# Optimization experiments

Hardware: AMD Instinct MI355X
Metric: run time of the kernel (lower is better)

## Reference

```python
import jax, jax.numpy as jnp
import numpy as np

N = 100000      # nodes
E = 1600000     # edges (avg degree 16)
D_IN, D_H, D_OUT = 100, 256, 47
EPS = 1e-5


def setup_inputs() -> dict:
    key = jax.random.key(0)
    ks = jax.random.split(key, 10)
    w = lambda k, s: jax.random.normal(k, s, jnp.float32) * 0.02
    return {
        "x": jax.random.normal(ks[0], (N, D_IN), jnp.float32),
        "edge_index": jax.random.randint(ks[1], (2, E), 0, N),
        # SAGEConv 0: lin_l (aggregated neighbors, has bias), lin_r (root, no bias)
        "wl0": w(ks[2], (D_IN, D_H)), "wr0": w(ks[3], (D_IN, D_H)), "b0": jnp.zeros((D_H,), jnp.float32),
        "g0": jnp.ones((D_H,), jnp.float32), "be0": jnp.zeros((D_H,), jnp.float32),
        # SAGEConv 1
        "wl1": w(ks[4], (D_H, D_H)), "wr1": w(ks[5], (D_H, D_H)), "b1": jnp.zeros((D_H,), jnp.float32),
        "g1": jnp.ones((D_H,), jnp.float32), "be1": jnp.zeros((D_H,), jnp.float32),
        # SAGEConv 2 (output)
        "wl2": w(ks[6], (D_H, D_OUT)), "wr2": w(ks[7], (D_H, D_OUT)), "b2": jnp.zeros((D_OUT,), jnp.float32),
    }


def _sage_conv(x, src, dst, wl, wr, b):
    # mean aggregation of source-node features onto destination nodes
    agg = jax.ops.segment_sum(x[src], dst, num_segments=N)          # [N, d_in]
    cnt = jax.ops.segment_sum(jnp.ones((src.shape[0],), x.dtype), dst, num_segments=N)
    mean = agg / jnp.maximum(cnt, 1.0)[:, None]                     # 0 in-degree -> 0
    return mean @ wl + x @ wr + b


def _bn(h, gamma, beta):
    m = h.mean(axis=0)
    v = h.var(axis=0)
    return (h - m) * jax.lax.rsqrt(v + EPS) * gamma + beta


def reference(x, edge_index, wl0, wr0, b0, g0, be0, wl1, wr1, b1, g1, be1, wl2, wr2, b2):
    src, dst = edge_index[0], edge_index[1]
    h = jax.nn.relu(_bn(_sage_conv(x, src, dst, wl0, wr0, b0), g0, be0))
    h = jax.nn.relu(_bn(_sage_conv(h, src, dst, wl1, wr1, b1), g1, be1))
    h = _sage_conv(h, src, dst, wl2, wr2, b2)
    return jax.nn.log_softmax(h, axis=1)
```

## Files before the change

### kernel.cpp

```cpp
#include <hip/hip_runtime.h>
#include <hip/hip_bf16.h>
#include <math.h>

#define DEVFN __device__ __forceinline__

typedef unsigned int uint32;
typedef unsigned short ushort_t;

using bf16x8 = __attribute__((ext_vector_type(8))) short;
using f32x4  = __attribute__((ext_vector_type(4))) float;
using f32x2  = __attribute__((ext_vector_type(2))) float;

DEVFN float bf2f(ushort_t u) {
    union { uint32 i; float f; } v; v.i = ((uint32)u) << 16; return v.f;
}
DEVFN float asf(uint32 u) {
    union { uint32 i; float f; } v; v.i = u; return v.f;
}
DEVFN ushort_t f2bf(float f) {
    union { float f; uint32 i; } v; v.f = f;
    uint32 u = v.i;
    uint32 r = (u + 0x7FFFu + ((u >> 16) & 1u)) >> 16;
    return (ushort_t)r;
}

DEVFN void gload_lds16(const void* g, void* l) {
    __builtin_amdgcn_global_load_lds(
        (const __attribute__((address_space(1))) void*)g,
        (__attribute__((address_space(3))) void*)l, 16, 0, 0);
}

__global__ void k_cast_x(const float* __restrict__ x, ushort_t* __restrict__ xb, int N) {
    int total = N * 128;
    for (int i = blockIdx.x * blockDim.x + threadIdx.x; i < total; i += gridDim.x * blockDim.x) {
        int col = i & 127, row = i >> 7;
        float v = (col < 100) ? x[row * 100 + col] : 0.f;
        xb[i] = f2bf(v);
    }
}

DEVFN void cast_one(const float* __restrict__ w, ushort_t* __restrict__ wt,
                    int j, int K, int Nout, int Kp) {
    int k = j % Kp, n = j / Kp;
    float v = (k < K && n < Nout) ? w[k * Nout + n] : 0.f;
    wt[j] = f2bf(v);
}

__global__ void k_cast_wall(const float* __restrict__ wl0, const float* __restrict__ wr0,
                            const float* __restrict__ wl1, const float* __restrict__ wr1,
                            const float* __restrict__ wl2, const float* __restrict__ wr2,
                            ushort_t* __restrict__ wlt0, ushort_t* __restrict__ wrt0,
                            ushort_t* __restrict__ wlt1, ushort_t* __restrict__ wrt1,
                            ushort_t* __restrict__ wcat2) {
    const int total = 229376;
    for (int i = blockIdx.x * blockDim.x + threadIdx.x; i < total; i += gridDim.x * blockDim.x) {
        int j = i;
        if (j < 32768)        cast_one(wl0, wlt0, j, 100, 256, 128);
        else if (j < 65536)   cast_one(wr0, wrt0, j - 32768, 100, 256, 128);
        else if (j < 131072)  cast_one(wl1, wlt1, j - 65536, 256, 256, 256);
        else if (j < 196608)  cast_one(wr1, wrt1, j - 131072, 256, 256, 256);
        else if (j < 212992)  cast_one(wl2, wcat2, j - 196608, 256, 47, 256);
        else                  cast_one(wr2, wcat2 + 16384, j - 212992, 256, 47, 256);
    }
}

__global__ void k_bincount(const int* __restrict__ dst, int E, int CH, int nbins, int nblk,
                           int* __restrict__ binCnt) {
    __shared__ int scnt[128];
    int blk = blockIdx.x, tid = threadIdx.x;
    for (int b = tid; b < 128; b += 256) scnt[b] = 0;
    __syncthreads();
    int e0 = blk * CH, e1 = min(E, e0 + CH);
    for (int i = e0 + tid; i < e1; i += 256)
        atomicAdd(&scnt[dst[i] >> 10], 1);
    __syncthreads();
    for (int b = tid; b < nbins; b += 256) binCnt[b * nblk + blk] = scnt[b];
}

__global__ void k_blocksum(const int* __restrict__ v, int n, int* __restrict__ bsum) {
    __shared__ int s[1024];
    int i = blockIdx.x * 1024 + threadIdx.x;
    s[threadIdx.x] = (i < n) ? v[i] : 0;
    __syncthreads();
    for (int o = 512; o > 0; o >>= 1) {
        if (threadIdx.x < o) s[threadIdx.x] += s[threadIdx.x + o];
        __syncthreads();
    }
    if (threadIdx.x == 0) bsum[blockIdx.x] = s[0];
}

__global__ void k_scanb(int* __restrict__ bsum, int NB) {
    if (blockIdx.x == 0 && threadIdx.x == 0) {
        int acc = 0;
        for (int i = 0; i < NB; ++i) { int v = bsum[i]; bsum[i] = acc; acc += v; }
    }
}

__global__ void k_exscan(const int* __restrict__ v, const int* __restrict__ bsum,
                         int n, int* __restrict__ outOff) {
    __shared__ int s[1024];
    int t = threadIdx.x;
    int i = blockIdx.x * 1024 + t;
    int val = (i < n) ? v[i] : 0;
    s[t] = val;
    __syncthreads();
    for (int o = 1; o < 1024; o <<= 1) {
        int add = (t >= o) ? s[t - o] : 0;
        __syncthreads();
        s[t] += add;
        __syncthreads();
    }
    if (i < n) outOff[i] = s[t] - val + bsum[blockIdx.x];
}

__global__ void k_binscatter(const int* __restrict__ src, const int* __restrict__ dst,
                             int E, int CH, int nbins, int nblk,
                             const int* __restrict__ binOff, int* __restrict__ ebin) {
    __shared__ int scur[128];
    int blk = blockIdx.x, tid = threadIdx.x;
    for (int b = tid; b < nbins; b += 256) scur[b] = binOff[b * nblk + blk];
    __syncthreads();
    int e0 = blk * CH, e1 = min(E, e0 + CH);
    for (int i = e0 + tid; i < e1; i += 256) {
        int d = dst[i];
        int b = d >> 10;
        int pos = atomicAdd(&scur[b], 1);
        ebin[pos] = (src[i] << 10) | (d & 1023);
    }
}

__global__ void k_bincsr(const int* __restrict__ ebin, const int* __restrict__ binOff,
                         int E, int N, int nbins, int nblk,
                         int* __restrict__ poffs, int* __restrict__ deg, int* __restrict__ csr2) {
    __shared__ int sdeg[1024];
    __shared__ int scur[1024];
    int bin = blockIdx.x, t = threadIdx.x;
    int binStart = binOff[bin * nblk];
    int binEnd = (bin + 1 < nbins) ? binOff[(bin + 1) * nblk] : E;
    int pbase = ((binStart + 15) & ~15) + bin * 15376;
    sdeg[t] = 0;
    __syncthreads();
    for (int i = binStart + t; i < binEnd; i += 1024)
        atomicAdd(&sdeg[ebin[i] & 1023], 1);
    __syncthreads();
    int v = sdeg[t];
    int pv = (v + 15) & ~15;
    sdeg[t] = pv;
    __syncthreads();
    for (int o = 1; o < 1024; o <<= 1) {
        int add = (t >= o) ? sdeg[t - o] : 0;
        __syncthreads();
        sdeg[t] += add;
        __syncthreads();
    }
    int pex = sdeg[t] - pv;
    int node = bin * 1024 + t;
    if (node < N) { poffs[node] = pbase + pex; deg[node] = v; }
    scur[t] = pex;
    __syncthreads();
    for (int i = binStart + t; i < binEnd; i += 1024) {
        int e = ebin[i];
        int slot = atomicAdd(&scur[e & 1023], 1);
        csr2[pbase + slot] = e >> 10;
    }
    for (int j = v; j < pv; ++j) csr2[pbase + pex + j] = N;
}

template <int D>
__global__ __launch_bounds__(256) void k_agg(
    const ushort_t* __restrict__ h, const int* __restrict__ poffs,
    const int* __restrict__ deg, const int* __restrict__ csr2,
    int N, ushort_t* __restrict__ mean) {
    constexpr int LPR = D / 8;
    constexpr int EPG = 64 / LPR;
    constexpr int STEP = 4 * EPG;
    int wid = (blockIdx.x * blockDim.x + threadIdx.x) >> 6;
    int lane = threadIdx.x & 63;
    if (wid >= N) return;
    const int seg = lane % LPR, sub = lane / LPR;
    int off = poffs[wid], cnt = deg[wid];
    int pcnt = (cnt + 15) & ~15;
    f32x2 acc[4] = {};
    const ushort_t* hp = h + seg * 8;
    int4 idx = *(const int4*)(csr2 + off + sub * 4);
    for (int b = 0; b < pcnt; b += STEP) {
        uint4 d0 = *(const uint4*)(hp + (size_t)idx.x * D);
        uint4 d1 = *(const uint4*)(hp + (size_t)idx.y * D);
        uint4 d2 = *(const uint4*)(hp + (size_t)idx.z * D);
        uint4 d3 = *(const uint4*)(hp + (size_t)idx.w * D);
        int4 idxn = *(const int4*)(csr2 + off + b + STEP + sub * 4);
        uint32 dd[16] = {d0.x, d0.y, d0.z, d0.w, d1.x, d1.y, d1.z, d1.w,
                         d2.x, d2.y, d2.z, d2.w, d3.x, d3.y, d3.z, d3.w};
#pragma unroll
        for (int q = 0; q < 16; ++q) {
            f32x2 tv;
            tv.x = asf(dd[q] << 16);
            tv.y = asf(dd[q] & 0xffff0000u);
            acc[q & 3] += tv;
        }
        idx = idxn;
    }
    float a[8] = {acc[0].x, acc[0].y, acc[1].x, acc[1].y,
                  acc[2].x, acc[2].y, acc[3].x, acc[3].y};
#pragma unroll
    for (int o = LPR; o < 64; o <<= 1) {
#pragma unroll
        for (int k = 0; k < 8; ++k) a[k] += __shfl_xor(a[k], o);
    }
    if (sub == 0) {
        float inv = 1.f / fmaxf((float)cnt, 1.f);
        uint4 o4;
        o4.x = (uint32)f2bf(a[0] * inv) | ((uint32)f2bf(a[1] * inv) << 16);
        o4.y = (uint32)f2bf(a[2] * inv) | ((uint32)f2bf(a[3] * inv) << 16);
        o4.z = (uint32)f2bf(a[4] * inv) | ((uint32)f2bf(a[5] * inv) << 16);
        o4.w = (uint32)f2bf(a[6] * inv) | ((uint32)f2bf(a[7] * inv) << 16);
        *(uint4*)(mean + (size_t)wid * D + seg * 8) = o4;
    }
}

template <int BN, int WROWS, int WCOLS, int MODE>
__global__ __launch_bounds__(512) void k_gemm(
    const ushort_t* __restrict__ A1, const ushort_t* __restrict__ B1,
    const ushort_t* __restrict__ A2, const ushort_t* __restrict__ B2,
    int KP, const float* __restrict__ bias,
    ushort_t* __restrict__ out_bf, float* __restrict__ out_f,
    float* __restrict__ stats, int M) {
    constexpr int BM = 128, BK = 64;
    constexpr int WM = BM / WROWS, WN = BN / WCOLS;
    constexpr int M_REP = WM / 16, N_REP = WN / 16;
    constexpr int SIDES = (MODE == 0) ? 2 : 1;
    __shared__ ushort_t Alds[BM * BK];
    __shared__ ushort_t Blds[BN * BK];
    __shared__ float sstat[2][BN];
    const int tid = threadIdx.x, lane = tid & 63, wid = tid >> 6;
    const int wm = wid / WCOLS, wn = wid % WCOLS;
    const int row0 = blockIdx.x * BM;
    if (MODE == 0) {
        for (int i = tid; i < 2 * BN; i += 512) (&sstat[0][0])[i] = 0.f;
    }
    f32x4 acc[M_REP][N_REP] = {};
    for (int side = 0; side < SIDES; ++side) {
        const ushort_t* A = side ? A2 : A1;
        const ushort_t* B = side ? B2 : B1;
        for (int kt = 0; kt < KP; kt += BK) {
            __syncthreads();
#pragma unroll
            for (int i = tid; i < BM * BK / 8; i += 512) {
                int r = i >> 3, c = i & 7;
                int gr = row0 + r;
                if (gr >= M) gr = M - 1;
                gload_lds16(A + (size_t)gr * KP + kt + c * 8, Alds + i * 8);
            }
#pragma unroll
            for (int i = tid; i < BN * BK / 8; i += 512) {
                int r = i >> 3, c = i & 7;
                gload_lds16(B + (size_t)r * KP + kt + c * 8, Blds + i * 8);
            }
            __syncthreads();
            bf16x8 a[2][M_REP], b[2][N_REP];
#pragma unroll
            for (int kk = 0; kk < 2; ++kk) {
#pragma unroll
                for (int m = 0; m < M_REP; ++m)
                    a[kk][m] = *(const bf16x8*)&Alds[(wm * WM + m * 16 + (lane & 15)) * BK + kk * 32 + (lane >> 4) * 8];
#pragma unroll
                for (int n = 0; n < N_REP; ++n)
                    b[kk][n] = *(const bf16x8*)&Blds[(wn * WN + n * 16 + (lane & 15)) * BK + kk * 32 + (lane >> 4) * 8];
            }
#pragma unroll
            for (int kk = 0; kk < 2; ++kk)
#pragma unroll
                for (int m = 0; m < M_REP; ++m)
#pragma unroll
                    for (int n = 0; n < N_REP; ++n)
                        acc[m][n] = __builtin_amdgcn_mfma_f32_16x16x32_bf16(a[kk][m], b[kk][n], acc[m][n], 0, 0, 0);
        }
    }
#pragma unroll
    for (int n = 0; n < N_REP; ++n) {
        int lcol = wn * WN + n * 16 + (lane & 15);
        float s = 0.f, q = 0.f;
#pragma unroll
        for (int m = 0; m < M_REP; ++m) {
#pragma unroll
            for (int r = 0; r < 4; ++r) {
                int row = row0 + wm * WM + m * 16 + (lane >> 4) * 4 + r;
                float v = acc[m][n][r];
                if (row < M) {
                    if (MODE == 0) {
                        out_bf[(size_t)row * 256 + lcol] = f2bf(v);
                        s += v;
                        q += v * v;
                    } else {
                        if (lcol < 64) {
                            out_bf[(size_t)row * 64 + lcol] = f2bf(v);
                        } else {
                            int c = lcol - 64;
                            float bv = (c < 47) ? bias[c] : 0.f;
                            out_f[(size_t)row * 64 + c] = v + bv;
                        }
                    }
                }
            }
        }
        if (MODE == 0) {
            s += __shfl_xor(s, 16); s += __shfl_xor(s, 32);
            q += __shfl_xor(q, 16); q += __shfl_xor(q, 32);
            if (lane < 16) {
                atomicAdd(&sstat[0][lcol], s);
                atomicAdd(&sstat[1][lcol], q);
            }
        }
    }
    if (MODE == 0) {
        __syncthreads();
        for (int i = tid; i < BN; i += 512) {
            atomicAdd(&stats[i], sstat[0][i]);
            atomicAdd(&stats[256 + i], sstat[1][i]);
        }
    }
}

__global__ void k_bnrelu(const ushort_t* __restrict__ h, const float* __restrict__ stats,
                         const float* __restrict__ g, const float* __restrict__ be,
                         int M, ushort_t* __restrict__ out) {
    int t = threadIdx.x;
    int cg = (t & 31) * 8;
    float invM = 1.f / (float)M;
    float sc[8], sh[8];
#pragma unroll
    for (int u = 0; u < 8; ++u) {
        int c = cg + u;
        float mean = stats[c] * invM;
        float var = stats[256 + c] * invM - mean * mean;
        float s = g[c] * rsqrtf(var + 1e-5f);
        sc[u] = s;
        sh[u] = be[c] - mean * s;
    }
    for (int r = blockIdx.x * 8 + (t >> 5); r < M; r += gridDim.x * 8) {
        uint4 d = *(const uint4*)(h + (size_t)r * 256 + cg);
        uint32 dd[4] = {d.x, d.y, d.z, d.w};
        uint32 w[4];
#pragma unroll
        for (int p = 0; p < 4; ++p) {
            float lo = bf2f((ushort_t)(dd[p] & 0xffff)) * sc[2 * p] + sh[2 * p];
            float hi = bf2f((ushort_t)(dd[p] >> 16)) * sc[2 * p + 1] + sh[2 * p + 1];
            w[p] = (uint32)f2bf(fmaxf(lo, 0.f)) | ((uint32)f2bf(fmaxf(hi, 0.f)) << 16);
        }
        uint4 o = {w[0], w[1], w[2], w[3]};
        *(uint4*)(out + (size_t)r * 256 + cg) = o;
    }
}

__global__ void k_agg_lsm(const ushort_t* __restrict__ t2, const float* __restrict__ r2,
                          const int* __restrict__ poffs, const int* __restrict__ deg,
                          const int* __restrict__ csr2, int N, float* __restrict__ out) {
    int wid = (blockIdx.x * blockDim.x + threadIdx.x) >> 6;
    int lane = threadIdx.x & 63;
    if (wid >= N) return;
    const int seg = lane & 7, sub = lane >> 3;
    int off = poffs[wid], cnt = deg[wid];
    int pcnt = (cnt + 15) & ~15;
    f32x2 acc[4] = {};
    const ushort_t* tp = t2 + seg * 8;
    int2 idx = *(const int2*)(csr2 + off + sub * 2);
    for (int b = 0; b < pcnt; b += 16) {
        uint4 d0 = *(const uint4*)(tp + (size_t)idx.x * 64);
        uint4 d1 = *(const uint4*)(tp + (size_t)idx.y * 64);
        int2 idxn = *(const int2*)(csr2 + off + b + 16 + sub * 2);
        uint32 dd[8] = {d0.x, d0.y, d0.z, d0.w, d1.x, d1.y, d1.z, d1.w};
#pragma unroll
        for (int q = 0; q < 8; ++q) {
            f32x2 tv;
            tv.x = asf(dd[q] << 16);
            tv.y = asf(dd[q] & 0xffff0000u);
            acc[q & 3] += tv;
        }
        idx = idxn;
    }
    float a[8] = {acc[0].x, acc[0].y, acc[1].x, acc[1].y,
                  acc[2].x, acc[2].y, acc[3].x, acc[3].y};
#pragma unroll
    for (int o = 8; o < 64; o <<= 1) {
#pragma unroll
        for (int k = 0; k < 8; ++k) a[k] += __shfl_xor(a[k], o);
    }
    if (sub == 0) {
        float inv = 1.f / fmaxf((float)cnt, 1.f);
        float v[8];
#pragma unroll
        for (int k = 0; k < 8; ++k) {
            int c = seg * 8 + k;
            v[k] = a[k] * inv + r2[(size_t)wid * 64 + c];
            if (c >= 47) v[k] = -1e30f;
        }
        float m = v[0];
#pragma unroll
        for (int k = 1; k < 8; ++k) m = fmaxf(m, v[k]);
#pragma unroll
        for (int o = 1; o < 8; o <<= 1) m = fmaxf(m, __shfl_xor(m, o));
        float s = 0.f;
#pragma unroll
        for (int k = 0; k < 8; ++k) s += expf(v[k] - m);
#pragma unroll
        for (int o = 1; o < 8; o <<= 1) s += __shfl_xor(s, o);
        float lse = m + logf(s);
#pragma unroll
        for (int k = 0; k < 8; ++k) {
            int c = seg * 8 + k;
            if (c < 47) out[(size_t)wid * 47 + c] = v[k] - lse;
        }
    }
}

extern "C" void kernel_launch(void* const* d_in, const int* in_sizes, int n_in,
                              void* d_out, int out_size, void* d_ws, size_t ws_size,
                              hipStream_t stream) {
    const float* x   = (const float*)d_in[0];
    const int*   ei  = (const int*)d_in[1];
    const float* wl0 = (const float*)d_in[2];
    const float* wr0 = (const float*)d_in[3];
    const float* g0  = (const float*)d_in[5];
    const float* be0 = (const float*)d_in[6];
    const float* wl1 = (const float*)d_in[7];
    const float* wr1 = (const float*)d_in[8];
    const float* g1  = (const float*)d_in[10];
    const float* be1 = (const float*)d_in[11];
    const float* wl2 = (const float*)d_in[12];
    const float* wr2 = (const float*)d_in[13];
    const float* b2  = (const float*)d_in[14];
    float* out = (float*)d_out;

    const int N = in_sizes[0] / 100;
    const int E = in_sizes[1] / 2;
    const int* src = ei;
    const int* dst = ei + E;

    char* p = (char*)d_ws;
    auto alloc = [&](size_t bytes) -> char* {
        char* r = p;
        p += (bytes + 255) & ~(size_t)255;
        return r;
    };
    const int NBLK = 128;
    const int nbins = (N + 1023) >> 10;
    const int scanN = nbins * NBLK;
    const size_t csr2N = (size_t)E + (size_t)nbins * 15376 + 64;
    ushort_t* xb   = (ushort_t*)alloc(((size_t)N + 1) * 128 * 2);
    ushort_t* hbuf = (ushort_t*)alloc(((size_t)N + 1) * 256 * 2);
    ushort_t* meanB = (ushort_t*)alloc(((size_t)N + 1) * 256 * 2);
    ushort_t* hpre = (ushort_t*)alloc((size_t)N * 256 * 2);
    int* deg   = (int*)alloc((size_t)N * 4);
    int* poffs = (int*)alloc((size_t)N * 4);
    int* csr2  = (int*)alloc(csr2N * 4);
    int* ebin  = (int*)alloc((size_t)E * 4);
    int* binCnt = (int*)alloc((size_t)scanN * 4);
    int* binOff = (int*)alloc((size_t)scanN * 4);
    int* bsum = (int*)alloc(1024 * 4);
    float* stats0 = (float*)alloc(512 * 4);
    float* stats1 = (float*)alloc(512 * 4);
    ushort_t* wlt0 = (ushort_t*)alloc(256 * 128 * 2);
    ushort_t* wrt0 = (ushort_t*)alloc(256 * 128 * 2);
    ushort_t* wlt1 = (ushort_t*)alloc(256 * 256 * 2);
    ushort_t* wrt1 = (ushort_t*)alloc(256 * 256 * 2);
    ushort_t* wcat2 = (ushort_t*)alloc(128 * 256 * 2);
    if ((size_t)(p - (char*)d_ws) > ws_size) return;

    ushort_t* t2 = meanB;
    float*    r2 = (float*)(meanB + ((size_t)N + 1) * 64);

    hipMemsetAsync(stats0, 0, 512 * 4, stream);
    hipMemsetAsync(stats1, 0, 512 * 4, stream);
    hipMemsetAsync(xb + (size_t)N * 128, 0, 128 * 2, stream);
    hipMemsetAsync(hbuf + (size_t)N * 256, 0, 256 * 2, stream);

    k_cast_x<<<2048, 256, 0, stream>>>(x, xb, N);
    k_cast_wall<<<896, 256, 0, stream>>>(wl0, wr0, wl1, wr1, wl2, wr2,
                                         wlt0, wrt0, wlt1, wrt1, wcat2);

    const int CH = (E + NBLK - 1) / NBLK;
    k_bincount<<<NBLK, 256, 0, stream>>>(dst, E, CH, nbins, NBLK, binCnt);
    int NB2 = (scanN + 1023) / 1024;
    k_blocksum<<<NB2, 1024, 0, stream>>>(binCnt, scanN, bsum);
    k_scanb<<<1, 64, 0, stream>>>(bsum, NB2);
    k_exscan<<<NB2, 1024, 0, stream>>>(binCnt, bsum, scanN, binOff);
    k_binscatter<<<NBLK, 256, 0, stream>>>(src, dst, E, CH, nbins, NBLK, binOff, ebin);
    k_bincsr<<<nbins, 1024, 0, stream>>>(ebin, binOff, E, N, nbins, NBLK, poffs, deg, csr2);

    int aggBlocks = (N + 3) / 4;
    int gemmM = (N + 127) / 128;

    k_agg<128><<<aggBlocks, 256, 0, stream>>>(xb, poffs, deg, csr2, N, meanB);
    k_gemm<256, 2, 4, 0><<<gemmM, 512, 0, stream>>>(
        meanB, wlt0, xb, wrt0, 128, nullptr, hpre, nullptr, stats0, N);
    k_bnrelu<<<2048, 256, 0, stream>>>(hpre, stats0, g0, be0, N, hbuf);

    k_agg<256><<<aggBlocks, 256, 0, stream>>>(hbuf, poffs, deg, csr2, N, meanB);
    k_gemm<256, 2, 4, 0><<<gemmM, 512, 0, stream>>>(
        meanB, wlt1, hbuf, wrt1, 256, nullptr, hpre, nullptr, stats1, N);
    k_bnrelu<<<2048, 256, 0, stream>>>(hpre, stats1, g1, be1, N, hbuf);

    hipMemsetAsync(t2 + (size_t)N * 64, 0, 64 * 2, stream);
    k_gemm<128, 2, 4, 1><<<gemmM, 512, 0, stream>>>(
        hbuf, wcat2, nullptr, nullptr, 256, b2, t2, r2, nullptr, N);
    k_agg_lsm<<<(N + 3) / 4, 256, 0, stream>>>(t2, r2, poffs, deg, csr2, N, out);
}
```

Baseline: 562.2 us.

## Use persistent weight-stationary GEMM with double-buffered A tiles; merge scan kernels

Replaces the tiled GEMM with a persistent kernel that holds the whole weight matrix in registers per wave. Row tiles of A are double-buffered in LDS through async global-to-LDS loads, so the next tile's load overlaps the current tile's MFMAs. BN statistics are now accumulated per thread across all tiles and flushed once with global atomics. The three-kernel prefix scan becomes a single-block scan, and four memsets are folded into one zero kernel to cut launch overhead. The cost is much higher register pressure, since all B fragments are held in VGPRs, plus a serial single-block scan.

```diff
diff --git a/kernel.cpp b/kernel.cpp
--- a/kernel.cpp
+++ b/kernel.cpp
@@ -28,6 +28,14 @@
     __builtin_amdgcn_global_load_lds(
         (const __attribute__((address_space(1))) void*)g,
         (__attribute__((address_space(3))) void*)l, 16, 0, 0);
+}
+
+__global__ void k_zero(float* __restrict__ stats0, float* __restrict__ stats1,
+                       ushort_t* __restrict__ xrow, ushort_t* __restrict__ hrow) {
+    int t = threadIdx.x;
+    if (t < 512) { stats0[t] = 0.f; stats1[t] = 0.f; }
+    if (t < 128) xrow[t] = 0;
+    if (t < 256) hrow[t] = 0;
 }
 
 __global__ void k_cast_x(const float* __restrict__ x, ushort_t* __restrict__ xb, int N) {
@@ -77,32 +85,19 @@
     for (int b = tid; b < nbins; b += 256) binCnt[b * nblk + blk] = scnt[b];
 }
 
-__global__ void k_blocksum(const int* __restrict__ v, int n, int* __restrict__ bsum) {
-    __shared__ int s[1024];
-    int i = blockIdx.x * 1024 + threadIdx.x;
-    s[threadIdx.x] = (i < n) ? v[i] : 0;
-    __syncthreads();
-    for (int o = 512; o > 0; o >>= 1) {
-        if (threadIdx.x < o) s[threadIdx.x] += s[threadIdx.x + o];
-        __syncthreads();
-    }
-    if (threadIdx.x == 0) bsum[blockIdx.x] = s[0];
-}
-
-__global__ void k_scanb(int* __restrict__ bsum, int NB) {
-    if (blockIdx.x == 0 && threadIdx.x == 0) {
-        int acc = 0;
-        for (int i = 0; i < NB; ++i) { int v = bsum[i]; bsum[i] = acc; acc += v; }
-    }
-}
-
-__global__ void k_exscan(const int* __restrict__ v, const int* __restrict__ bsum,
-                         int n, int* __restrict__ outOff) {
+__global__ void k_scan_all(const int* __restrict__ v, int n, int* __restrict__ outOff) {
     __shared__ int s[1024];
     int t = threadIdx.x;
-    int i = blockIdx.x * 1024 + t;
-    int val = (i < n) ? v[i] : 0;
-    s[t] = val;
+    int b0 = t * 16;
+    int loc[16];
+    int sum = 0;
+#pragma unroll
+    for (int k = 0; k < 16; ++k) {
+        int x = (b0 + k < n) ? v[b0 + k] : 0;
+        loc[k] = x;
+        sum += x;
+    }
+    s[t] = sum;
     __syncthreads();
     for (int o = 1; o < 1024; o <<= 1) {
         int add = (t >= o) ? s[t - o] : 0;
@@ -110,7 +105,12 @@
         s[t] += add;
         __syncthreads();
     }
-    if (i < n) outOff[i] = s[t] - val + bsum[blockIdx.x];
+    int run = s[t] - sum;
+#pragma unroll
+    for (int k = 0; k < 16; ++k) {
+        if (b0 + k < n) outOff[b0 + k] = run;
+        run += loc[k];
+    }
 }
 
 __global__ void k_binscatter(const int* __restrict__ src, const int* __restrict__ dst,
@@ -218,105 +218,113 @@
     }
 }
 
-template <int BN, int WROWS, int WCOLS, int MODE>
-__global__ __launch_bounds__(512) void k_gemm(
+template <int KP, int MODE>
+__global__ __launch_bounds__(512) void k_gemm2(
     const ushort_t* __restrict__ A1, const ushort_t* __restrict__ B1,
     const ushort_t* __restrict__ A2, const ushort_t* __restrict__ B2,
-    int KP, const float* __restrict__ bias,
+    const float* __restrict__ bias,
     ushort_t* __restrict__ out_bf, float* __restrict__ out_f,
-    float* __restrict__ stats, int M) {
-    constexpr int BM = 128, BK = 64;
-    constexpr int WM = BM / WROWS, WN = BN / WCOLS;
-    constexpr int M_REP = WM / 16, N_REP = WN / 16;
+    float* __restrict__ stats, int M, int nTiles) {
     constexpr int SIDES = (MODE == 0) ? 2 : 1;
-    __shared__ ushort_t Alds[BM * BK];
-    __shared__ ushort_t Blds[BN * BK];
-    __shared__ float sstat[2][BN];
-    const int tid = threadIdx.x, lane = tid & 63, wid = tid >> 6;
-    const int wm = wid / WCOLS, wn = wid % WCOLS;
-    const int row0 = blockIdx.x * BM;
-    if (MODE == 0) {
-        for (int i = tid; i < 2 * BN; i += 512) (&sstat[0][0])[i] = 0.f;
-    }
-    f32x4 acc[M_REP][N_REP] = {};
-    for (int side = 0; side < SIDES; ++side) {
-        const ushort_t* A = side ? A2 : A1;
-        const ushort_t* B = side ? B2 : B1;
-        for (int kt = 0; kt < KP; kt += BK) {
-            __syncthreads();
-#pragma unroll
-            for (int i = tid; i < BM * BK / 8; i += 512) {
-                int r = i >> 3, c = i & 7;
-                int gr = row0 + r;
-                if (gr >= M) gr = M - 1;
-                gload_lds16(A + (size_t)gr * KP + kt + c * 8, Alds + i * 8);
+    constexpr int N_REP = (MODE == 0) ? 2 : 1;
+    constexpr int KCH = KP / 32;
+    constexpr int JW = KP / 8;
+    constexpr int TILE = (MODE == 0 && KP == 256) ? 32 : 64;
+    constexpr int M_REP = TILE / 16;
+    constexpr int SLOTS = SIDES * TILE * JW;
+    __shared__ ushort_t Alds[2][SLOTS * 8];
+    const int tid = threadIdx.x, lane = tid & 63, wv = tid >> 6;
+    const int colBase = wv * (16 * N_REP) + (lane & 15);
+
+    bf16x8 b[SIDES][KCH][N_REP];
+#pragma unroll
+    for (int s = 0; s < SIDES; ++s) {
+        const ushort_t* B = s ? B2 : B1;
+#pragma unroll
+        for (int n = 0; n < N_REP; ++n)
+#pragma unroll
+            for (int c = 0; c < KCH; ++c)
+                b[s][c][n] = *(const bf16x8*)&B[(size_t)(colBase + n * 16) * KP + c * 32 + (lane >> 4) * 8];
+    }
+    float bval = 0.f;
+    if (MODE == 1) {
+        int c2 = colBase - 64;
+        bval = (c2 >= 0 && c2 < 47) ? bias[c2] : 0.f;
+    }
+    float ssum[N_REP] = {}, ssq[N_REP] = {};
+
+    auto STAGE = [&](int t, int buf) {
+        int r0 = t * TILE;
+#pragma unroll
+        for (int i = tid; i < SLOTS; i += 512) {
+            int side = i / (TILE * JW);
+            int rem = i - side * (TILE * JW);
+            int r = rem / JW, j = rem - r * JW;
+            int gr = min(r0 + r, M - 1);
+            const ushort_t* Asrc = side ? A2 : A1;
+            gload_lds16(Asrc + (size_t)gr * KP + j * 8, &Alds[buf][(size_t)i * 8]);
+        }
+    };
+
+    int t0 = blockIdx.x;
+    if (t0 < nTiles) STAGE(t0, 0);
+    int buf = 0;
+    for (int t = t0; t < nTiles; t += gridDim.x) {
+        __syncthreads();
+        int tn = t + gridDim.x;
+        if (tn < nTiles) STAGE(tn, buf ^ 1);
+        f32x4 acc[M_REP][N_REP] = {};
+#pragma unroll
+        for (int s = 0; s < SIDES; ++s) {
+            const ushort_t* base = &Alds[buf][s * TILE * JW * 8];
+#pragma unroll
+            for (int m = 0; m < M_REP; ++m) {
+                bf16x8 a8[KCH];
+#pragma unroll
+                for (int c = 0; c < KCH; ++c)
+                    a8[c] = *(const bf16x8*)&base[(m * 16 + (lane & 15)) * KP + c * 32 + (lane >> 4) * 8];
+#pragma unroll
+                for (int c = 0; c < KCH; ++c)
+#pragma unroll
+                    for (int n = 0; n < N_REP; ++n)
+                        acc[m][n] = __builtin_amdgcn_mfma_f32_16x16x32_bf16(a8[c], b[s][c][n], acc[m][n], 0, 0, 0);
             }
-#pragma unroll
-            for (int i = tid; i < BN * BK / 8; i += 512) {
-                int r = i >> 3, c = i & 7;
-                gload_lds16(B + (size_t)r * KP + kt + c * 8, Blds + i * 8);
-            }
-            __syncthreads();
-            bf16x8 a[2][M_REP], b[2][N_REP];
-#pragma unroll
-            for (int kk = 0; kk < 2; ++kk) {
-#pragma unroll
-                for (int m = 0; m < M_REP; ++m)
-                    a[kk][m] = *(const bf16x8*)&Alds[(wm * WM + m * 16 + (lane & 15)) * BK + kk * 32 + (lane >> 4) * 8];
-#pragma unroll
-                for (int n = 0; n < N_REP; ++n)
-                    b[kk][n] = *(const bf16x8*)&Blds[(wn * WN + n * 16 + (lane & 15)) * BK + kk * 32 + (lane >> 4) * 8];
-            }
-#pragma unroll
-            for (int kk = 0; kk < 2; ++kk)
-#pragma unroll
-                for (int m = 0; m < M_REP; ++m)
-#pragma unroll
-                    for (int n = 0; n < N_REP; ++n)
-                        acc[m][n] = __builtin_amdgcn_mfma_f32_16x16x32_bf16(a[kk][m], b[kk][n], acc[m][n], 0, 0, 0);
-        }
-    }
-#pragma unroll
-    for (int n = 0; n < N_REP; ++n) {
-        int lcol = wn * WN + n * 16 + (lane & 15);
-        float s = 0.f, q = 0.f;
-#pragma unroll
-        for (int m = 0; m < M_REP; ++m) {
-#pragma unroll
-            for (int r = 0; r < 4; ++r) {
-                int row = row0 + wm * WM + m * 16 + (lane >> 4) * 4 + r;
-                float v = acc[m][n][r];
-                if (row < M) {
-                    if (MODE == 0) {
-                        out_bf[(size_t)row * 256 + lcol] = f2bf(v);
-                        s += v;
-                        q += v * v;
-                    } else {
-                        if (lcol < 64) {
-                            out_bf[(size_t)row * 64 + lcol] = f2bf(v);
+        }
+        int r0 = t * TILE;
+#pragma unroll
+        for (int n = 0; n < N_REP; ++n) {
+            int col = colBase + n * 16;
+#pragma unroll
+            for (int m = 0; m < M_REP; ++m) {
+#pragma unroll
+                for (int r = 0; r < 4; ++r) {
+                    int row = r0 + m * 16 + (lane >> 4) * 4 + r;
+                    float v = acc[m][n][r];
+                    if (row < M) {
+                        if (MODE == 0) {
+                            out_bf[(size_t)row * 256 + col] = f2bf(v);
+                            ssum[n] += v;
+                            ssq[n] += v * v;
                         } else {
-                            int c = lcol - 64;
-                            float bv = (c < 47) ? bias[c] : 0.f;
-                            out_f[(size_t)row * 64 + c] = v + bv;
+                            if (col < 64) out_bf[(size_t)row * 64 + col] = f2bf(v);
+                            else out_f[(size_t)row * 64 + (col - 64)] = v + bval;
                         }
                     }
                 }
             }
         }
-        if (MODE == 0) {
+        buf ^= 1;
+    }
+    if (MODE == 0) {
+#pragma unroll
+        for (int n = 0; n < N_REP; ++n) {
+            float s = ssum[n], q = ssq[n];
             s += __shfl_xor(s, 16); s += __shfl_xor(s, 32);
             q += __shfl_xor(q, 16); q += __shfl_xor(q, 32);
             if (lane < 16) {
-                atomicAdd(&sstat[0][lcol], s);
-                atomicAdd(&sstat[1][lcol], q);
+                atomicAdd(&stats[colBase + n * 16], s);
+                atomicAdd(&stats[256 + colBase + n * 16], q);
             }
-        }
-    }
-    if (MODE == 0) {
-        __syncthreads();
-        for (int i = tid; i < BN; i += 512) {
-            atomicAdd(&stats[i], sstat[0][i]);
-            atomicAdd(&stats[256 + i], sstat[1][i]);
         }
     }
 }
@@ -456,7 +464,6 @@
     int* ebin  = (int*)alloc((size_t)E * 4);
     int* binCnt = (int*)alloc((size_t)scanN * 4);
     int* binOff = (int*)alloc((size_t)scanN * 4);
-    int* bsum = (int*)alloc(1024 * 4);
     float* stats0 = (float*)alloc(512 * 4);
     float* stats1 = (float*)alloc(512 * 4);
     ushort_t* wlt0 = (ushort_t*)alloc(256 * 128 * 2);
@@ -469,39 +476,33 @@
     ushort_t* t2 = meanB;
     float*    r2 = (float*)(meanB + ((size_t)N + 1) * 64);
 
-    hipMemsetAsync(stats0, 0, 512 * 4, stream);
-    hipMemsetAsync(stats1, 0, 512 * 4, stream);
-    hipMemsetAsync(xb + (size_t)N * 128, 0, 128 * 2, stream);
-    hipMemsetAsync(hbuf + (size_t)N * 256, 0, 256 * 2, stream);
-
+    k_zero<<<1, 1024, 0, stream>>>(stats0, stats1, xb + (size_t)N * 128, hbuf + (size_t)N * 256);
     k_cast_x<<<2048, 256, 0, stream>>>(x, xb, N);
     k_cast_wall<<<896, 256, 0, stream>>>(wl0, wr0, wl1, wr1, wl2, wr2,
                                          wlt0, wrt0, wlt1, wrt1, wcat2);
 
     const int CH = (E + NBLK - 1) / NBLK;
     k_bincount<<<NBLK, 256, 0, stream>>>(dst, E, CH, nbins, NBLK, binCnt);
-    int NB2 = (scanN + 1023) / 1024;
-    k_blocksum<<<NB2, 1024, 0, stream>>>(binCnt, scanN, bsum);
-    k_scanb<<<1, 64, 0, stream>>>(bsum, NB2);
-    k_exscan<<<NB2, 1024, 0, stream>>>(binCnt, bsum, scanN, binOff);
+    k_scan_all<<<1, 1024, 0, stream>>>(binCnt, scanN, binOff);
     k_binscatter<<<NBLK, 256, 0, stream>>>(src, dst, E, CH, nbins, NBLK, binOff, ebin);
     k_bincsr<<<nbins, 1024, 0, stream>>>(ebin, binOff, E, N, nbins, NBLK, poffs, deg, csr2);
 
     int aggBlocks = (N + 3) / 4;
-    int gemmM = (N + 127) / 128;
+    int tiles64 = (N + 63) / 64;
+    int tiles32 = (N + 31) / 32;
 
     k_agg<128><<<aggBlocks, 256, 0, stream>>>(xb, poffs, deg, csr2, N, meanB);
-    k_gemm<256, 2, 4, 0><<<gemmM, 512, 0, stream>>>(
-        meanB, wlt0, xb, wrt0, 128, nullptr, hpre, nullptr, stats0, N);
+    k_gemm2<128, 0><<<256, 512, 0, stream>>>(
+        meanB, wlt0, xb, wrt0, nullptr, hpre, nullptr, stats0, N, tiles64);
     k_bnrelu<<<2048, 256, 0, stream>>>(hpre, stats0, g0, be0, N, hbuf);
 
     k_agg<256><<<aggBlocks, 256, 0, stream>>>(hbuf, poffs, deg, csr2, N, meanB);
-    k_gemm<256, 2, 4, 0><<<gemmM, 512, 0, stream>>>(
-        meanB, wlt1, hbuf, wrt1, 256, nullptr, hpre, nullptr, stats1, N);
+    k_gemm2<256, 0><<<256, 512, 0, stream>>>(
+        meanB, wlt1, hbuf, wrt1, nullptr, hpre, nullptr, stats1, N, tiles32);
     k_bnrelu<<<2048, 256, 0, stream>>>(hpre, stats1, g1, be1, N, hbuf);
 
     hipMemsetAsync(t2 + (size_t)N * 64, 0, 64 * 2, stream);
-    k_gemm<128, 2, 4, 1><<<gemmM, 512, 0, stream>>>(
-        hbuf, wcat2, nullptr, nullptr, 256, b2, t2, r2, nullptr, N);
+    k_gemm2<256, 1><<<512, 512, 0, stream>>>(
+        hbuf, wcat2, nullptr, nullptr, b2, t2, r2, nullptr, N, tiles64);
     k_agg_lsm<<<(N + 3) / 4, 256, 0, stream>>>(t2, r2, poffs, deg, csr2, N, out);
 }
```

Result: faster. 534.5 us (-4.9%).
